# Performance work log

Hardware: AMD Instinct MI355X
Metric: run time of the kernel (lower is better)

The kernel has to match this reference:

```python
import jax, jax.numpy as jnp
import numpy as np

N_DST = 25000
E = 400000
DN = 128   # dim_node
DE = 128   # dim_edge
DT = 128   # dim_time
DO = 128   # dim_out
H = 2      # num_head


def setup_inputs() -> dict:
    key = jax.random.key(0)
    ks = jax.random.split(key, 10)
    sc = 0.05
    node_h = jax.random.normal(ks[0], (N_DST + E, DN), jnp.float32)
    edge_f = jax.random.normal(ks[1], (E, DE), jnp.float32)
    dt = jax.random.uniform(ks[2], (E,), jnp.float32) * 100.0
    dst_idx = jax.random.randint(ks[3], (E,), 0, N_DST)
    # TimeEncode: Linear(1, dim_time) with w initialized to 1/10**linspace(0,9)
    time_w = jnp.asarray(1.0 / 10 ** np.linspace(0, 9, DT, dtype=np.float32))
    time_b = jnp.zeros((DT,), jnp.float32)
    Wq = jax.random.normal(ks[4], (DO, DN + DT), jnp.float32) * sc
    bq = jnp.zeros((DO,), jnp.float32)
    Wk = jax.random.normal(ks[5], (DO, DN + DE + DT), jnp.float32) * sc
    bk = jnp.zeros((DO,), jnp.float32)
    Wv = jax.random.normal(ks[6], (DO, DN + DE + DT), jnp.float32) * sc
    bv = jnp.zeros((DO,), jnp.float32)
    Wout = jax.random.normal(ks[7], (DO, DN + DO), jnp.float32) * sc
    bout = jnp.zeros((DO,), jnp.float32)
    gamma = jnp.ones((DO,), jnp.float32)
    beta = jnp.zeros((DO,), jnp.float32)
    return dict(node_h=node_h, edge_f=edge_f, dt=dt, dst_idx=dst_idx,
                time_w=time_w, time_b=time_b, Wq=Wq, bq=bq, Wk=Wk, bk=bk,
                Wv=Wv, bv=bv, Wout=Wout, bout=bout, gamma=gamma, beta=beta)


def reference(node_h, edge_f, dt, dst_idx, time_w, time_b,
              Wq, bq, Wk, bk, Wv, bv, Wout, bout, gamma, beta):
    num_dst = node_h.shape[0] - edge_f.shape[0]
    num_edges = edge_f.shape[0]
    tgt = node_h[:num_dst]            # [N, DN] target node embeddings
    src = node_h[num_dst:]            # [E, DN] per-edge source embeddings

    # TimeEncode: cos(w * dt + b)
    time_feats = jnp.cos(dt[:, None] * time_w[None, :] + time_b)          # [E, DT]
    zero_time = jnp.broadcast_to(jnp.cos(time_b), (num_dst, time_b.shape[0]))

    Qn = jnp.concatenate([tgt, zero_time], axis=1) @ Wq.T + bq            # [N, DO]
    kv_in = jnp.concatenate([src, edge_f, time_feats], axis=1)            # [E, DN+DE+DT]
    K = kv_in @ Wk.T + bk                                                 # [E, DO]
    V = kv_in @ Wv.T + bv                                                 # [E, DO]
    Q = Qn[dst_idx]                                                       # gather per edge

    d_head = Q.shape[1] // H
    Qh = Q.reshape(num_edges, H, d_head)
    Kh = K.reshape(num_edges, H, d_head)
    Vh = V.reshape(num_edges, H, d_head)

    score = jnp.sum(Qh * Kh, axis=2)                                      # [E, H]
    score = jnp.where(score >= 0, score, 0.2 * score)                     # LeakyReLU(0.2)

    # edge_softmax: segmented softmax over incoming edges of each dst node
    m = jax.ops.segment_max(score, dst_idx, num_segments=num_dst)
    m = jnp.where(jnp.isfinite(m), m, 0.0)                                # empty segments
    e = jnp.exp(score - m[dst_idx])
    s = jax.ops.segment_sum(e, dst_idx, num_segments=num_dst)
    att = e / s[dst_idx]                                                  # [E, H]

    Vw = (Vh * att[:, :, None]).reshape(num_edges, -1)                    # [E, DO]
    h = jax.ops.segment_sum(Vw, dst_idx, num_segments=num_dst)            # scatter-sum

    rst = jnp.concatenate([h, tgt], axis=1) @ Wout.T + bout               # [N, DO]
    rst = jax.nn.relu(rst)
    mu = jnp.mean(rst, axis=-1, keepdims=True)
    var = jnp.var(rst, axis=-1, keepdims=True)
    return (rst - mu) / jnp.sqrt(var + 1e-5) * gamma + beta
```

## Files before the change

kernel.cpp:

```cpp
#include <hip/hip_runtime.h>

#define N_DST 25000
#define E_NUM 400000

typedef __bf16 bf16x8 __attribute__((ext_vector_type(8)));
typedef __bf16 bf16x4 __attribute__((ext_vector_type(4)));
typedef __bf16 bf16x2 __attribute__((ext_vector_type(2)));
typedef float  f32x4  __attribute__((ext_vector_type(4)));

__device__ __forceinline__ float fast_cos(float x) {
  float r = x * 0.15915494309189535f;
  r = r - floorf(r);
  return __builtin_amdgcn_cosf(r);
}

__global__ __launch_bounds__(128) void cq_kernel(const float* __restrict__ Wq,
    const float* __restrict__ bq, const float* __restrict__ tb, float* __restrict__ cq) {
  int o = threadIdx.x;
  float s = bq[o];
  for (int j = 0; j < 128; ++j) s += cosf(tb[j]) * Wq[o * 256 + 128 + j];
  cq[o] = s;
}

__global__ __launch_bounds__(256) void pack_kernel(const float* __restrict__ W0,
    const float* __restrict__ W1, int srcStride, int N, int total, __bf16* __restrict__ Bp) {
  int idx = blockIdx.x * 256 + threadIdx.x;
  if (idx >= total) return;
  int g = idx / N, n = idx - g * N;
  const float* src = (W1 && n >= 128) ? (W1 + (size_t)(n - 128) * srcStride)
                                      : (W0 + (size_t)n * srcStride);
  const float4* s4 = reinterpret_cast<const float4*>(src + g * 8);
  float4 lo = s4[0], hi = s4[1];
  bf16x8 b;
  b[0] = (__bf16)lo.x; b[1] = (__bf16)lo.y; b[2] = (__bf16)lo.z; b[3] = (__bf16)lo.w;
  b[4] = (__bf16)hi.x; b[5] = (__bf16)hi.y; b[6] = (__bf16)hi.z; b[7] = (__bf16)hi.w;
  reinterpret_cast<bf16x8*>(Bp)[idx] = b;
}

__global__ __launch_bounds__(256) void count_kernel(const int* __restrict__ dsti, int* __restrict__ counts) {
  int e = blockIdx.x * 256 + threadIdx.x;
  if (e < E_NUM) atomicAdd(&counts[dsti[e]], 1);
}

__global__ __launch_bounds__(1024) void scan_kernel(const int* __restrict__ counts,
    int* __restrict__ offs, int* __restrict__ cursor) {
  __shared__ int wpart[16];
  int tid = threadIdx.x, lane = tid & 63, wid = tid >> 6;
  int carry = 0;
  for (int base = 0; base < N_DST; base += 1024) {
    int idx = base + tid;
    int x = (idx < N_DST) ? counts[idx] : 0;
    int incl = x;
#pragma unroll
    for (int o = 1; o < 64; o <<= 1) {
      int y = __shfl_up(incl, o);
      if (lane >= o) incl += y;
    }
    if (lane == 63) wpart[wid] = incl;
    __syncthreads();
    if (wid == 0) {
      int v = (lane < 16) ? wpart[lane] : 0;
      int s = v;
#pragma unroll
      for (int o = 1; o < 16; o <<= 1) {
        int y = __shfl_up(s, o);
        if (lane >= o) s += y;
      }
      if (lane < 16) wpart[lane] = s;
    }
    __syncthreads();
    int woff = (wid > 0) ? wpart[wid - 1] : 0;
    int tot = wpart[15];
    if (idx < N_DST) {
      int v = carry + woff + incl - x;
      offs[idx] = v;
      cursor[idx] = v;
    }
    carry += tot;
    __syncthreads();
  }
  if (tid == 0) offs[N_DST] = carry;
}

__global__ __launch_bounds__(256) void fill_kernel(const int* __restrict__ dsti,
    int* __restrict__ cursor, int* __restrict__ elist, int* __restrict__ dsts) {
  int e = blockIdx.x * 256 + threadIdx.x;
  if (e < E_NUM) {
    int d = dsti[e];
    int p = atomicAdd(&cursor[d], 1);
    elist[p] = e;
    dsts[p] = d;
  }
}

template<int MODE>
__global__ __launch_bounds__(256) void gemm_kernel(
    const float* __restrict__ A0, const float* __restrict__ A1,
    const float* __restrict__ dtp, const float* __restrict__ tw, const float* __restrict__ tb,
    const __bf16* __restrict__ Bp,
    const float* __restrict__ bias0, const float* __restrict__ bias1,
    const int* __restrict__ elist, const int* __restrict__ dsts,
    const float* __restrict__ Qn,
    float* __restrict__ outF, __bf16* __restrict__ Vout, float* __restrict__ score)
{
  constexpr int KD = (MODE == 0) ? 128 : ((MODE == 1) ? 384 : 256);
  constexpr int NC = (MODE == 1) ? 256 : 128;
  constexpr int KB = KD * 2;
  constexpr int NFRAG = NC / 64;
  __shared__ __align__(16) char Atile[64 * KB];
  __shared__ int Elds[64];
  __shared__ int Dlds[64];
  __shared__ float dts[64];
  __shared__ float twl[128];
  __shared__ float tbl[128];

  const int tid = threadIdx.x;
  const int e0 = blockIdx.x * 64;
  const int nv = (MODE == 1) ? 64 : min(64, N_DST - e0);

  if constexpr (MODE == 1) {
    if (tid < 64) {
      int e = elist[e0 + tid];
      Elds[tid] = e;
      Dlds[tid] = dsts[e0 + tid];
      dts[tid] = dtp[e];
    } else if (tid < 192) {
      int j = tid - 64;
      twl[j] = tw[j];
      tbl[j] = tb[j];
    }
    __syncthreads();
    float4 sv[8], ev[8];
#pragma unroll
    for (int i = 0; i < 8; ++i) {
      int c = tid + i * 256;
      int r = c >> 5, c4 = (c & 31) << 2;
      int eidx = Elds[r];
      sv[i] = *reinterpret_cast<const float4*>(A0 + ((size_t)N_DST + eidx) * 128 + c4);
      ev[i] = *reinterpret_cast<const float4*>(A1 + (size_t)eidx * 128 + c4);
    }
#pragma unroll
    for (int i = 0; i < 16; ++i) {
      int c2 = tid + i * 256;
      int r = c2 >> 6, j = (c2 & 63) << 1;
      float d = dts[r];
      bf16x2 p;
      p[0] = (__bf16)fast_cos(d * twl[j] + tbl[j]);
      p[1] = (__bf16)fast_cos(d * twl[j + 1] + tbl[j + 1]);
      *reinterpret_cast<bf16x2*>(Atile + r * KB + ((512 + j * 2) ^ ((r & 7) << 4))) = p;
    }
#pragma unroll
    for (int i = 0; i < 8; ++i) {
      int c = tid + i * 256;
      int r = c >> 5, c4 = (c & 31) << 2;
      bf16x4 b0, b1;
      b0[0] = (__bf16)sv[i].x; b0[1] = (__bf16)sv[i].y; b0[2] = (__bf16)sv[i].z; b0[3] = (__bf16)sv[i].w;
      b1[0] = (__bf16)ev[i].x; b1[1] = (__bf16)ev[i].y; b1[2] = (__bf16)ev[i].z; b1[3] = (__bf16)ev[i].w;
      *reinterpret_cast<bf16x4*>(Atile + r * KB + ((c4 * 2) ^ ((r & 7) << 4))) = b0;
      *reinterpret_cast<bf16x4*>(Atile + r * KB + ((256 + c4 * 2) ^ ((r & 7) << 4))) = b1;
    }
    __syncthreads();
  } else {
#pragma unroll
    for (int i = 0; i < 8; ++i) {
      int c = tid + i * 256;
      int r = c >> 5, c4 = (c & 31) << 2;
      float4 v0 = make_float4(0.f, 0.f, 0.f, 0.f);
      float4 v1 = make_float4(0.f, 0.f, 0.f, 0.f);
      if (r < nv) {
        v0 = *reinterpret_cast<const float4*>(A0 + (size_t)(e0 + r) * 128 + c4);
        if constexpr (MODE == 2)
          v1 = *reinterpret_cast<const float4*>(A1 + (size_t)(e0 + r) * 128 + c4);
      }
      bf16x4 b0;
      b0[0] = (__bf16)v0.x; b0[1] = (__bf16)v0.y; b0[2] = (__bf16)v0.z; b0[3] = (__bf16)v0.w;
      *reinterpret_cast<bf16x4*>(Atile + r * KB + ((c4 * 2) ^ ((r & 7) << 4))) = b0;
      if constexpr (MODE == 2) {
        bf16x4 b1;
        b1[0] = (__bf16)v1.x; b1[1] = (__bf16)v1.y; b1[2] = (__bf16)v1.z; b1[3] = (__bf16)v1.w;
        *reinterpret_cast<bf16x4*>(Atile + r * KB + ((256 + c4 * 2) ^ ((r & 7) << 4))) = b1;
      }
    }
    __syncthreads();
  }

  const int lane = tid & 63;
  const int w = tid >> 6;
  const int nbase = w * (NC / 4);
  const int lrow = lane & 15;
  const int lk = lane >> 4;
  const int aswz = (lrow & 7) << 4;

  f32x4 acc[4][NFRAG];
#pragma unroll
  for (int mf = 0; mf < 4; ++mf)
#pragma unroll
    for (int nf = 0; nf < NFRAG; ++nf)
      acc[mf][nf] = (f32x4){0.f, 0.f, 0.f, 0.f};

#pragma unroll
  for (int kk = 0; kk < KD; kk += 32) {
    bf16x8 b[NFRAG];
#pragma unroll
    for (int nf = 0; nf < NFRAG; ++nf)
      b[nf] = reinterpret_cast<const bf16x8*>(Bp)[((kk >> 3) + lk) * NC + nbase + nf * 16 + lrow];
    bf16x8 a[4];
#pragma unroll
    for (int mf = 0; mf < 4; ++mf)
      a[mf] = *reinterpret_cast<const bf16x8*>(
          Atile + (mf * 16 + lrow) * KB + (((kk + lk * 8) * 2) ^ aswz));
#pragma unroll
    for (int nf = 0; nf < NFRAG; ++nf)
#pragma unroll
      for (int mf = 0; mf < 4; ++mf)
        acc[mf][nf] = __builtin_amdgcn_mfma_f32_16x16x32_bf16(a[mf], b[nf], acc[mf][nf], 0, 0, 0);
  }

  if constexpr (MODE != 1) {
#pragma unroll
    for (int nf = 0; nf < NFRAG; ++nf) {
      int col = nbase + nf * 16 + lrow;
      float bb = bias0[col];
#pragma unroll
      for (int mf = 0; mf < 4; ++mf) {
#pragma unroll
        for (int r = 0; r < 4; ++r) {
          int row = mf * 16 + lk * 4 + r;
          if (row < nv) {
            float val = acc[mf][nf][r] + bb;
            if constexpr (MODE == 2) val = fmaxf(val, 0.f);
            outF[(size_t)(e0 + row) * 128 + col] = val;
          }
        }
      }
    }
  } else {
    __syncthreads();
    if (w >= 2) {
#pragma unroll
      for (int nf = 0; nf < 4; ++nf) {
        int vcol = (nbase - 128) + nf * 16 + lrow;
        float bb = bias1[vcol];
#pragma unroll
        for (int mf = 0; mf < 4; ++mf) {
#pragma unroll
          for (int r = 0; r < 4; ++r) {
            int row = mf * 16 + lk * 4 + r;
            *reinterpret_cast<__bf16*>(Atile + row * 256 + ((vcol * 2) ^ ((row & 7) << 4))) =
                (__bf16)(acc[mf][nf][r] + bb);
          }
        }
      }
    } else {
      float bkv[4];
#pragma unroll
      for (int nf = 0; nf < 4; ++nf) bkv[nf] = bias0[w * 64 + nf * 16 + lrow];
#pragma unroll
      for (int mf = 0; mf < 4; ++mf) {
#pragma unroll
        for (int r = 0; r < 4; ++r) {
          int row = mf * 16 + lk * 4 + r;
          const float* qrow = Qn + ((size_t)Dlds[row] << 7) + w * 64;
          float s = 0.f;
#pragma unroll
          for (int nf = 0; nf < 4; ++nf)
            s += (acc[mf][nf][r] + bkv[nf]) * qrow[nf * 16 + lrow];
          s += __shfl_xor(s, 1);
          s += __shfl_xor(s, 2);
          s += __shfl_xor(s, 4);
          s += __shfl_xor(s, 8);
          if (lrow == 0) {
            s = (s >= 0.f) ? s : 0.2f * s;
            score[((size_t)(e0 + row) << 1) + w] = s;
          }
        }
      }
    }
    __syncthreads();
#pragma unroll
    for (int i = 0; i < 4; ++i) {
      int c = tid + i * 256;
      int r = c >> 4, cb = (c & 15) << 4;
      bf16x8 v = *reinterpret_cast<const bf16x8*>(Atile + r * 256 + (cb ^ ((r & 7) << 4)));
      *reinterpret_cast<bf16x8*>(Vout + (((size_t)(e0 + r)) << 7) + (c & 15) * 8) = v;
    }
  }
}

__global__ __launch_bounds__(64) void agg_kernel(const int* __restrict__ offs,
    const float* __restrict__ score, const __bf16* __restrict__ V, float* __restrict__ h) {
  int d = blockIdx.x;
  int lane = threadIdx.x;
  int beg = offs[d], end = offs[d + 1];
  int n = end - beg;
  float m0 = -3.0e38f, m1 = -3.0e38f;
  for (int i = lane; i < n; i += 64) {
    float2 sc = *reinterpret_cast<const float2*>(score + 2 * (size_t)(beg + i));
    m0 = fmaxf(m0, sc.x); m1 = fmaxf(m1, sc.y);
  }
#pragma unroll
  for (int o = 32; o; o >>= 1) {
    m0 = fmaxf(m0, __shfl_xor(m0, o));
    m1 = fmaxf(m1, __shfl_xor(m1, o));
  }
  float s0 = 0.f, s1 = 0.f;
  for (int i = lane; i < n; i += 64) {
    float2 sc = *reinterpret_cast<const float2*>(score + 2 * (size_t)(beg + i));
    s0 += __expf(sc.x - m0); s1 += __expf(sc.y - m1);
  }
#pragma unroll
  for (int o = 32; o; o >>= 1) {
    s0 += __shfl_xor(s0, o);
    s1 += __shfl_xor(s1, o);
  }
  float inv0 = (n > 0) ? 1.f / s0 : 0.f;
  float inv1 = (n > 0) ? 1.f / s1 : 0.f;
  int q = lane >> 4, j = lane & 15;
  int hsel = j >> 3;
  float acc[8];
#pragma unroll
  for (int k2 = 0; k2 < 8; ++k2) acc[k2] = 0.f;
  for (int i0 = 0; i0 < n; i0 += 4) {
    int i = i0 + q;
    if (i < n) {
      size_t p = beg + i;
      float2 sc = *reinterpret_cast<const float2*>(score + 2 * p);
      float wgt = hsel ? __expf(sc.y - m1) * inv1 : __expf(sc.x - m0) * inv0;
      bf16x8 v = *reinterpret_cast<const bf16x8*>(V + (p << 7) + j * 8);
#pragma unroll
      for (int k2 = 0; k2 < 8; ++k2) acc[k2] += wgt * (float)v[k2];
    }
  }
#pragma unroll
  for (int k2 = 0; k2 < 8; ++k2) {
    acc[k2] += __shfl_xor(acc[k2], 16);
    acc[k2] += __shfl_xor(acc[k2], 32);
  }
  if (q == 0) {
    float4 lo = make_float4(acc[0], acc[1], acc[2], acc[3]);
    float4 hi = make_float4(acc[4], acc[5], acc[6], acc[7]);
    float* dst = h + ((size_t)d << 7) + j * 8;
    *reinterpret_cast<float4*>(dst) = lo;
    *reinterpret_cast<float4*>(dst + 4) = hi;
  }
}

__global__ __launch_bounds__(256) void ln_kernel(const float* __restrict__ rst,
    const float* __restrict__ gamma, const float* __restrict__ beta, float* __restrict__ out) {
  int row = blockIdx.x * 4 + (threadIdx.x >> 6);
  int lane = threadIdx.x & 63;
  float2 v = *reinterpret_cast<const float2*>(rst + (size_t)row * 128 + lane * 2);
  float sum = v.x + v.y;
  float sq = v.x * v.x + v.y * v.y;
#pragma unroll
  for (int o = 32; o; o >>= 1) {
    sum += __shfl_xor(sum, o);
    sq  += __shfl_xor(sq, o);
  }
  float mean = sum * (1.f / 128.f);
  float var = sq * (1.f / 128.f) - mean * mean;
  float rs = rsqrtf(var + 1e-5f);
  float2 g = *reinterpret_cast<const float2*>(gamma + lane * 2);
  float2 b = *reinterpret_cast<const float2*>(beta + lane * 2);
  float2 o2;
  o2.x = (v.x - mean) * rs * g.x + b.x;
  o2.y = (v.y - mean) * rs * g.y + b.y;
  *reinterpret_cast<float2*>(out + (size_t)row * 128 + lane * 2) = o2;
}

extern "C" void kernel_launch(void* const* d_in, const int* in_sizes, int n_in,
                              void* d_out, int out_size, void* d_ws, size_t ws_size,
                              hipStream_t stream) {
  (void)in_sizes; (void)n_in; (void)out_size; (void)ws_size;
  const float* node_h = (const float*)d_in[0];
  const float* edge_f = (const float*)d_in[1];
  const float* dtp    = (const float*)d_in[2];
  const int*   dsti   = (const int*)d_in[3];
  const float* tw     = (const float*)d_in[4];
  const float* tb     = (const float*)d_in[5];
  const float* Wq     = (const float*)d_in[6];
  const float* bq     = (const float*)d_in[7];
  const float* Wk     = (const float*)d_in[8];
  const float* bk     = (const float*)d_in[9];
  const float* Wv     = (const float*)d_in[10];
  const float* bv     = (const float*)d_in[11];
  const float* Wout   = (const float*)d_in[12];
  const float* bout   = (const float*)d_in[13];
  const float* gamma  = (const float*)d_in[14];
  const float* beta   = (const float*)d_in[15];
  float* outp = (float*)d_out;

  size_t off = 0;
  auto take = [&](size_t nbytes) -> void* {
    void* r = (char*)d_ws + off;
    off += (nbytes + 255) & ~(size_t)255;
    return r;
  };
  __bf16* Bp_kv  = (__bf16*)take((size_t)48 * 256 * 8 * 2);
  __bf16* Bp_q   = (__bf16*)take((size_t)16 * 128 * 8 * 2);
  __bf16* Bp_out = (__bf16*)take((size_t)32 * 128 * 8 * 2);
  float*  cq     = (float*)take(128 * 4);
  float*  Qn     = (float*)take((size_t)N_DST * 128 * 4);
  __bf16* Vbuf   = (__bf16*)take((size_t)E_NUM * 128 * 2);
  float*  score  = (float*)take((size_t)E_NUM * 2 * 4);
  int*    counts = (int*)take((size_t)N_DST * 4);
  int*    offs   = (int*)take((size_t)(N_DST + 1) * 4);
  int*    cursor = (int*)take((size_t)N_DST * 4);
  int*    elist  = (int*)take((size_t)E_NUM * 4);
  int*    dsts   = (int*)take((size_t)E_NUM * 4);
  float*  hbuf   = (float*)take((size_t)N_DST * 128 * 4);
  float*  rst    = (float*)take((size_t)N_DST * 128 * 4);

  hipMemsetAsync(counts, 0, (size_t)N_DST * 4, stream);

  cq_kernel<<<1, 128, 0, stream>>>(Wq, bq, tb, cq);
  pack_kernel<<<(48 * 256 + 255) / 256, 256, 0, stream>>>(Wk, Wv, 384, 256, 48 * 256, Bp_kv);
  pack_kernel<<<(16 * 128 + 255) / 256, 256, 0, stream>>>(Wq, nullptr, 256, 128, 16 * 128, Bp_q);
  pack_kernel<<<(32 * 128 + 255) / 256, 256, 0, stream>>>(Wout, nullptr, 256, 128, 32 * 128, Bp_out);

  count_kernel<<<(E_NUM + 255) / 256, 256, 0, stream>>>(dsti, counts);
  scan_kernel<<<1, 1024, 0, stream>>>(counts, offs, cursor);
  fill_kernel<<<(E_NUM + 255) / 256, 256, 0, stream>>>(dsti, cursor, elist, dsts);

  gemm_kernel<0><<<(N_DST + 63) / 64, 256, 0, stream>>>(node_h, nullptr, nullptr, nullptr, nullptr,
      Bp_q, cq, nullptr, nullptr, nullptr, nullptr, Qn, nullptr, nullptr);
  gemm_kernel<1><<<E_NUM / 64, 256, 0, stream>>>(node_h, edge_f, dtp, tw, tb,
      Bp_kv, bk, bv, elist, dsts, Qn, nullptr, Vbuf, score);

  agg_kernel<<<N_DST, 64, 0, stream>>>(offs, score, Vbuf, hbuf);

  gemm_kernel<2><<<(N_DST + 63) / 64, 256, 0, stream>>>(hbuf, node_h, nullptr, nullptr, nullptr,
      Bp_out, bout, nullptr, nullptr, nullptr, nullptr, rst, nullptr, nullptr);
  ln_kernel<<<N_DST / 4, 256, 0, stream>>>(rst, gamma, beta, outp);
}
```

Measured before the change: 403.9 us.

## Fuse LayerNorm into output GEMM, pipeline MFMA operand loads, pack agg blocks

The ReLU+LayerNorm epilogue moves into the MODE 2 GEMM, with a cross-wave reduction through shared memory. This removes the separate ln kernel and the round trip of the rst buffer. The MFMA k-loop now prefetches B fragments three stages ahead and A fragments double-buffered to hide load latency. Launch bounds now request 3 waves per SIMD, and the time-encode fill is reorganised so each thread handles one row. agg_kernel packs four destination nodes per 256-thread block, and the higher register pressure may cause spills.

```diff
diff --git a/kernel.cpp b/kernel.cpp
--- a/kernel.cpp
+++ b/kernel.cpp
@@ -94,7 +94,7 @@
 }
 
 template<int MODE>
-__global__ __launch_bounds__(256) void gemm_kernel(
+__global__ __launch_bounds__(256, 3) void gemm_kernel(
     const float* __restrict__ A0, const float* __restrict__ A1,
     const float* __restrict__ dtp, const float* __restrict__ tw, const float* __restrict__ tb,
     const __bf16* __restrict__ Bp,
@@ -107,6 +107,7 @@
   constexpr int NC = (MODE == 1) ? 256 : 128;
   constexpr int KB = KD * 2;
   constexpr int NFRAG = NC / 64;
+  constexpr int NK = KD / 32;
   __shared__ __align__(16) char Atile[64 * KB];
   __shared__ int Elds[64];
   __shared__ int Dlds[64];
@@ -139,15 +140,23 @@
       sv[i] = *reinterpret_cast<const float4*>(A0 + ((size_t)N_DST + eidx) * 128 + c4);
       ev[i] = *reinterpret_cast<const float4*>(A1 + (size_t)eidx * 128 + c4);
     }
-#pragma unroll
-    for (int i = 0; i < 16; ++i) {
-      int c2 = tid + i * 256;
-      int r = c2 >> 6, j = (c2 & 63) << 1;
+    {
+      int r = tid >> 2;
+      int j0 = (tid & 3) << 5;
       float d = dts[r];
-      bf16x2 p;
-      p[0] = (__bf16)fast_cos(d * twl[j] + tbl[j]);
-      p[1] = (__bf16)fast_cos(d * twl[j + 1] + tbl[j + 1]);
-      *reinterpret_cast<bf16x2*>(Atile + r * KB + ((512 + j * 2) ^ ((r & 7) << 4))) = p;
+      char* rowb = Atile + r * KB;
+      int swz = (r & 7) << 4;
+      const float2* tw2 = reinterpret_cast<const float2*>(twl);
+      const float2* tb2 = reinterpret_cast<const float2*>(tbl);
+#pragma unroll
+      for (int i = 0; i < 16; ++i) {
+        int j = j0 + i * 2;
+        float2 wv = tw2[j >> 1], bv = tb2[j >> 1];
+        bf16x2 p;
+        p[0] = (__bf16)fast_cos(d * wv.x + bv.x);
+        p[1] = (__bf16)fast_cos(d * wv.y + bv.y);
+        *reinterpret_cast<bf16x2*>(rowb + ((512 + j * 2) ^ swz)) = p;
+      }
     }
 #pragma unroll
     for (int i = 0; i < 8; ++i) {
@@ -198,25 +207,36 @@
     for (int nf = 0; nf < NFRAG; ++nf)
       acc[mf][nf] = (f32x4){0.f, 0.f, 0.f, 0.f};
 
-#pragma unroll
-  for (int kk = 0; kk < KD; kk += 32) {
-    bf16x8 b[NFRAG];
+  const bf16x8* Bb = reinterpret_cast<const bf16x8*>(Bp) + (size_t)lk * NC + nbase + lrow;
+  bf16x8 bq[3][NFRAG];
+  bf16x8 aq[2][4];
+  auto loadB = [&](int ks) {
 #pragma unroll
     for (int nf = 0; nf < NFRAG; ++nf)
-      b[nf] = reinterpret_cast<const bf16x8*>(Bp)[((kk >> 3) + lk) * NC + nbase + nf * 16 + lrow];
-    bf16x8 a[4];
+      bq[ks % 3][nf] = Bb[(size_t)ks * 4 * NC + nf * 16];
+  };
+  auto loadA = [&](int ks) {
 #pragma unroll
     for (int mf = 0; mf < 4; ++mf)
-      a[mf] = *reinterpret_cast<const bf16x8*>(
-          Atile + (mf * 16 + lrow) * KB + (((kk + lk * 8) * 2) ^ aswz));
+      aq[ks % 2][mf] = *reinterpret_cast<const bf16x8*>(
+          Atile + (mf * 16 + lrow) * KB + (((ks * 32 + lk * 8) * 2) ^ aswz));
+  };
+  loadB(0);
+  if (NK > 1) loadB(1);
+  loadA(0);
+#pragma unroll
+  for (int ks = 0; ks < NK; ++ks) {
+    if (ks + 2 < NK) loadB(ks + 2);
+    if (ks + 1 < NK) loadA(ks + 1);
 #pragma unroll
     for (int nf = 0; nf < NFRAG; ++nf)
 #pragma unroll
       for (int mf = 0; mf < 4; ++mf)
-        acc[mf][nf] = __builtin_amdgcn_mfma_f32_16x16x32_bf16(a[mf], b[nf], acc[mf][nf], 0, 0, 0);
-  }
-
-  if constexpr (MODE != 1) {
+        acc[mf][nf] = __builtin_amdgcn_mfma_f32_16x16x32_bf16(aq[ks % 2][mf], bq[ks % 3][nf],
+                                                              acc[mf][nf], 0, 0, 0);
+  }
+
+  if constexpr (MODE == 0) {
 #pragma unroll
     for (int nf = 0; nf < NFRAG; ++nf) {
       int col = nbase + nf * 16 + lrow;
@@ -226,10 +246,68 @@
 #pragma unroll
         for (int r = 0; r < 4; ++r) {
           int row = mf * 16 + lk * 4 + r;
+          if (row < nv)
+            outF[(size_t)(e0 + row) * 128 + col] = acc[mf][nf][r] + bb;
+        }
+      }
+    }
+  } else if constexpr (MODE == 2) {
+    const float* gammaP = dtp;
+    const float* betaP = tw;
+    float vals[2][4][4];
+#pragma unroll
+    for (int nf = 0; nf < 2; ++nf) {
+      float bb = bias0[nbase + nf * 16 + lrow];
+#pragma unroll
+      for (int mf = 0; mf < 4; ++mf)
+#pragma unroll
+        for (int r = 0; r < 4; ++r)
+          vals[nf][mf][r] = fmaxf(acc[mf][nf][r] + bb, 0.f);
+    }
+    __syncthreads();
+    float* sums = reinterpret_cast<float*>(Atile);
+    float* sqs  = reinterpret_cast<float*>(Atile) + 256;
+    float* stats = reinterpret_cast<float*>(Atile) + 512;
+#pragma unroll
+    for (int mf = 0; mf < 4; ++mf) {
+#pragma unroll
+      for (int r = 0; r < 4; ++r) {
+        float s1 = vals[0][mf][r] + vals[1][mf][r];
+        float s2 = vals[0][mf][r] * vals[0][mf][r] + vals[1][mf][r] * vals[1][mf][r];
+#pragma unroll
+        for (int o = 1; o < 16; o <<= 1) {
+          s1 += __shfl_xor(s1, o);
+          s2 += __shfl_xor(s2, o);
+        }
+        if (lrow == 0) {
+          int row = mf * 16 + lk * 4 + r;
+          sums[w * 64 + row] = s1;
+          sqs[w * 64 + row] = s2;
+        }
+      }
+    }
+    __syncthreads();
+    if (tid < 64) {
+      float s = sums[tid] + sums[64 + tid] + sums[128 + tid] + sums[192 + tid];
+      float q = sqs[tid] + sqs[64 + tid] + sqs[128 + tid] + sqs[192 + tid];
+      float mean = s * (1.f / 128.f);
+      float var = q * (1.f / 128.f) - mean * mean;
+      stats[tid * 2] = mean;
+      stats[tid * 2 + 1] = rsqrtf(var + 1e-5f);
+    }
+    __syncthreads();
+#pragma unroll
+    for (int nf = 0; nf < 2; ++nf) {
+      int col = nbase + nf * 16 + lrow;
+      float g = gammaP[col], b = betaP[col];
+#pragma unroll
+      for (int mf = 0; mf < 4; ++mf) {
+#pragma unroll
+        for (int r = 0; r < 4; ++r) {
+          int row = mf * 16 + lk * 4 + r;
           if (row < nv) {
-            float val = acc[mf][nf][r] + bb;
-            if constexpr (MODE == 2) val = fmaxf(val, 0.f);
-            outF[(size_t)(e0 + row) * 128 + col] = val;
+            float mean = stats[row * 2], rs = stats[row * 2 + 1];
+            outF[(size_t)(e0 + row) * 128 + col] = (vals[nf][mf][r] - mean) * rs * g + b;
           }
         }
       }
@@ -287,10 +365,11 @@
   }
 }
 
-__global__ __launch_bounds__(64) void agg_kernel(const int* __restrict__ offs,
+__global__ __launch_bounds__(256) void agg_kernel(const int* __restrict__ offs,
     const float* __restrict__ score, const __bf16* __restrict__ V, float* __restrict__ h) {
-  int d = blockIdx.x;
-  int lane = threadIdx.x;
+  int d = blockIdx.x * 4 + (threadIdx.x >> 6);
+  if (d >= N_DST) return;
+  int lane = threadIdx.x & 63;
   int beg = offs[d], end = offs[d + 1];
   int n = end - beg;
   float m0 = -3.0e38f, m1 = -3.0e38f;
@@ -343,29 +422,6 @@
     *reinterpret_cast<float4*>(dst) = lo;
     *reinterpret_cast<float4*>(dst + 4) = hi;
   }
-}
-
-__global__ __launch_bounds__(256) void ln_kernel(const float* __restrict__ rst,
-    const float* __restrict__ gamma, const float* __restrict__ beta, float* __restrict__ out) {
-  int row = blockIdx.x * 4 + (threadIdx.x >> 6);
-  int lane = threadIdx.x & 63;
-  float2 v = *reinterpret_cast<const float2*>(rst + (size_t)row * 128 + lane * 2);
-  float sum = v.x + v.y;
-  float sq = v.x * v.x + v.y * v.y;
-#pragma unroll
-  for (int o = 32; o; o >>= 1) {
-    sum += __shfl_xor(sum, o);
-    sq  += __shfl_xor(sq, o);
-  }
-  float mean = sum * (1.f / 128.f);
-  float var = sq * (1.f / 128.f) - mean * mean;
-  float rs = rsqrtf(var + 1e-5f);
-  float2 g = *reinterpret_cast<const float2*>(gamma + lane * 2);
-  float2 b = *reinterpret_cast<const float2*>(beta + lane * 2);
-  float2 o2;
-  o2.x = (v.x - mean) * rs * g.x + b.x;
-  o2.y = (v.y - mean) * rs * g.y + b.y;
-  *reinterpret_cast<float2*>(out + (size_t)row * 128 + lane * 2) = o2;
 }
 
 extern "C" void kernel_launch(void* const* d_in, const int* in_sizes, int n_in,
@@ -409,7 +465,6 @@
   int*    elist  = (int*)take((size_t)E_NUM * 4);
   int*    dsts   = (int*)take((size_t)E_NUM * 4);
   float*  hbuf   = (float*)take((size_t)N_DST * 128 * 4);
-  float*  rst    = (float*)take((size_t)N_DST * 128 * 4);
 
   hipMemsetAsync(counts, 0, (size_t)N_DST * 4, stream);
 
@@ -427,9 +482,8 @@
   gemm_kernel<1><<<E_NUM / 64, 256, 0, stream>>>(node_h, edge_f, dtp, tw, tb,
       Bp_kv, bk, bv, elist, dsts, Qn, nullptr, Vbuf, score);
 
-  agg_kernel<<<N_DST, 64, 0, stream>>>(offs, score, Vbuf, hbuf);
-
-  gemm_kernel<2><<<(N_DST + 63) / 64, 256, 0, stream>>>(hbuf, node_h, nullptr, nullptr, nullptr,
-      Bp_out, bout, nullptr, nullptr, nullptr, nullptr, rst, nullptr, nullptr);
-  ln_kernel<<<N_DST / 4, 256, 0, stream>>>(rst, gamma, beta, outp);
-}
+  agg_kernel<<<(N_DST + 3) / 4, 256, 0, stream>>>(offs, score, Vbuf, hbuf);
+
+  gemm_kernel<2><<<(N_DST + 63) / 64, 256, 0, stream>>>(hbuf, node_h, gamma, beta, nullptr,
+      Bp_out, bout, nullptr, nullptr, nullptr, nullptr, outp, nullptr, nullptr);
+}
```

Result: faster. 368.9 us (-8.7%).
